# Optimization experiments

Hardware: AMD Instinct MI355X
Metric: run time of the kernel (lower is better)

The kernel has to match this reference:

```python
import jax, jax.numpy as jnp
import numpy as np

B, D = 32768, 1024


def setup_inputs() -> dict:
    key = jax.random.key(0)
    kx, k1, k2, k3 = jax.random.split(key, 4)
    x = jax.random.normal(kx, (B, D), dtype=jnp.float32)
    w1 = jax.random.normal(k1, (D, D), dtype=jnp.float32) * 0.1
    w2 = jax.random.normal(k2, (D, D), dtype=jnp.float32) * 0.1
    w3 = jax.random.normal(k3, (D, D), dtype=jnp.float32) * 0.1
    return {"x": x, "w1": w1, "w2": w2, "w3": w3}


def reference(x, w1, w2, w3):
    # Order 1: plain dense projection
    r1 = jnp.matmul(x, w1)  # [B, D]

    dim = x.shape[1]
    k = int(dim * 0.1)
    # Select top-k facets by mean |x| over the batch
    _, idx = jax.lax.top_k(jnp.abs(x).mean(axis=0), k)  # [k]
    mask = jnp.zeros((dim,), dtype=x.dtype).at[idx].set(1.0)  # [D]

    x_sparse = x * mask  # [B, D], zero outside active facets
    # Order 2: masked matmul, gated elementwise by the sparse input
    r2 = jnp.matmul(x_sparse, w2) * x_sparse
    # Order 3: masked matmul squared, gated elementwise
    r3 = jnp.square(jnp.matmul(x_sparse, w3)) * x_sparse
    return (r1, r2, r3)
```

## Files before the change

kernel.cpp:

```cpp
#include <hip/hip_runtime.h>
#include <hip/hip_bf16.h>
#include <stdint.h>

#define B_ROWS 32768
#define DIM    1024
#define KACT   102
#define KPAD   104

typedef short bf16x8 __attribute__((ext_vector_type(8)));
typedef unsigned short u16x8 __attribute__((ext_vector_type(8)));
typedef float f32x4  __attribute__((ext_vector_type(4)));

__device__ __forceinline__ unsigned short f2bf(float f) {
  union { float f; unsigned u; } v; v.f = f;
  unsigned u = v.u;
  unsigned r = u + 0x7fffu + ((u >> 16) & 1u);
  return (unsigned short)(r >> 16);
}
__device__ __forceinline__ float bfasf(unsigned hi16) {
  union { unsigned u; float f; } v; v.u = hi16;
  return v.f;
}

#define GLDS(g, l) __builtin_amdgcn_global_load_lds( \
    (__attribute__((address_space(1))) void*)(g),    \
    (__attribute__((address_space(3))) void*)(l), 16, 0, 0)

__global__ __launch_bounds__(256) void k_convw(
    const float* __restrict__ x, const float* __restrict__ w1,
    unsigned short* __restrict__ xb, unsigned short* __restrict__ w1t,
    float* __restrict__ partial) {
  const int t = threadIdx.x;
  if (blockIdx.x < 512) {
    const int c0 = t * 4;
    const size_t base = (size_t)blockIdx.x * 64 * DIM;
    float s0 = 0.f, s1 = 0.f, s2 = 0.f, s3 = 0.f;
    #pragma unroll 4
    for (int j = 0; j < 64; ++j) {
      size_t off = base + (size_t)j * DIM + c0;
      float4 v = *(const float4*)(x + off);
      s0 += fabsf(v.x); s1 += fabsf(v.y); s2 += fabsf(v.z); s3 += fabsf(v.w);
      ushort4 o;
      o.x = f2bf(v.x); o.y = f2bf(v.y); o.z = f2bf(v.z); o.w = f2bf(v.w);
      *(ushort4*)(xb + off) = o;
    }
    float4 p; p.x = s0; p.y = s1; p.z = s2; p.w = s3;
    *(float4*)(partial + (size_t)blockIdx.x * DIM + c0) = p;
  } else {
    __shared__ unsigned short tile[64][65];
    const int b  = blockIdx.x - 512;
    const int bx = b & 15;
    const int by = b >> 4;
    for (int e = t; e < 64 * 64; e += 256) {
      int r = e >> 6, c = e & 63;
      tile[r][c] = f2bf(w1[(size_t)(by * 64 + r) * DIM + bx * 64 + c]);
    }
    __syncthreads();
    for (int e = t; e < 64 * 64; e += 256) {
      int c = e >> 6, r = e & 63;
      w1t[(size_t)(bx * 64 + c) * DIM + by * 64 + r] = tile[r][c];
    }
  }
}

__global__ __launch_bounds__(128) void k_reduce1(const float* __restrict__ partial,
                                                 float* __restrict__ p2) {
  const int c  = (blockIdx.x & 7) * 128 + threadIdx.x;
  const int ks = blockIdx.x >> 3;
  float s = 0.f;
  #pragma unroll 8
  for (int p = ks * 64; p < ks * 64 + 64; ++p) s += partial[(size_t)p * DIM + c];
  p2[ks * DIM + c] = s;
}

__global__ __launch_bounds__(1024) void k_sel(const float* __restrict__ p2,
                                              int* __restrict__ act,
                                              int* __restrict__ cmap) {
  __shared__ double sv[DIM];
  __shared__ int wcnt[16];
  const int d = threadIdx.x;
  {
    double s = 0.0;
    #pragma unroll
    for (int ks = 0; ks < 8; ++ks) s += (double)p2[ks * DIM + d];
    sv[d] = s;
  }
  __syncthreads();
  const double sd = sv[d];
  int rank = 0;
  for (int j = 0; j < DIM; ++j) {
    double s = sv[j];
    rank += (s > sd || (s == sd && j < d)) ? 1 : 0;
  }
  const int f = (rank < KACT) ? 1 : 0;
  unsigned long long m = __ballot(f != 0);
  const int lane = d & 63, w = d >> 6;
  if (lane == 0) wcnt[w] = __popcll(m);
  __syncthreads();
  int off = 0;
  for (int i = 0; i < w; ++i) off += wcnt[i];
  int pos = off + __popcll(m & ((1ull << lane) - 1ull));
  cmap[d] = f ? pos : -1;
  if (f) act[pos] = d;
}

__global__ __launch_bounds__(128) void k_wsub(const float* __restrict__ w2,
                                              const float* __restrict__ w3,
                                              const int* __restrict__ act,
                                              float* __restrict__ W2sub,
                                              float* __restrict__ W3sub) {
  const int i = blockIdx.x;
  const int j = threadIdx.x;
  if (j >= KPAD) return;
  float v2 = 0.f, v3 = 0.f;
  if (i < KACT && j < KACT) {
    size_t o = (size_t)act[i] * DIM + act[j];
    v2 = w2[o]; v3 = w3[o];
  }
  W2sub[i * KPAD + j] = v2;
  W3sub[i * KPAD + j] = v3;
}

#define VMW8 asm volatile("s_waitcnt vmcnt(8)" ::: "memory")
#define VMW4 asm volatile("s_waitcnt vmcnt(4)" ::: "memory")
#define VMW0 asm volatile("s_waitcnt vmcnt(0)" ::: "memory")
#define NOP_ (void)0

#define STAGE_A(KT) do { \
  GLDS(Abase + (size_t)sr0 * 1024 + (KT) * 32 + sc0 * 8, &Asl[((KT)&3)*8192 + p0*8]); \
  GLDS(Abase + (size_t)sr1 * 1024 + (KT) * 32 + sc1 * 8, &Asl[((KT)&3)*8192 + p1*8]); \
} while (0)
#define STAGE_B(KT) do { \
  GLDS(Bbase + (size_t)sr0 * 1024 + (KT) * 32 + sc0 * 8, &Bsl[((KT)&3)*8192 + p0*8]); \
  GLDS(Bbase + (size_t)sr1 * 1024 + (KT) * 32 + sc1 * 8, &Bsl[((KT)&3)*8192 + p1*8]); \
} while (0)

#define PH0(SLOT, STAGE_STMT) do { \
  _Pragma("unroll") for (int i = 0; i < 4; ++i) \
    areg[i] = *(const bf16x8*)(&Asl[(SLOT)*8192 + aoff0 + i * 512]); \
  _Pragma("unroll") for (int i = 0; i < 4; ++i) \
    breg[i] = *(const bf16x8*)(&Bsl[(SLOT)*8192 + boff0 + i * 512]); \
  STAGE_STMT; \
  __builtin_amdgcn_s_barrier(); \
  __builtin_amdgcn_s_setprio(1); \
  _Pragma("unroll") for (int mi = 0; mi < 4; ++mi) \
  _Pragma("unroll") for (int ni = 0; ni < 4; ++ni) \
    acc[mi][ni] = __builtin_amdgcn_mfma_f32_16x16x32_bf16(areg[mi], breg[ni], acc[mi][ni], 0, 0, 0); \
  __builtin_amdgcn_s_setprio(0); \
  __builtin_amdgcn_s_barrier(); \
} while (0)

#define PH1(SLOT, STAGE_STMT, WAIT_STMT) do { \
  _Pragma("unroll") for (int i = 0; i < 4; ++i) \
    areg[i] = *(const bf16x8*)(&Asl[(SLOT)*8192 + aoff0 + 2048 + i * 512]); \
  STAGE_STMT; \
  WAIT_STMT; \
  __builtin_amdgcn_s_barrier(); \
  __builtin_amdgcn_s_setprio(1); \
  _Pragma("unroll") for (int mi = 0; mi < 4; ++mi) \
  _Pragma("unroll") for (int ni = 0; ni < 4; ++ni) \
    acc[4 + mi][ni] = __builtin_amdgcn_mfma_f32_16x16x32_bf16(areg[mi], breg[ni], acc[4 + mi][ni], 0, 0, 0); \
  __builtin_amdgcn_s_setprio(0); \
  __builtin_amdgcn_s_barrier(); \
} while (0)

__global__ __launch_bounds__(512, 1) void k_gemm_r1(
    const unsigned short* __restrict__ A,
    const unsigned short* __restrict__ Bt,
    float* __restrict__ C) {
  __shared__ unsigned short Asl[4 * 8192];
  __shared__ unsigned short Bsl[4 * 8192];

  const int t    = threadIdx.x;
  const int lane = t & 63;
  const int wave = t >> 6;
  const int wm   = wave >> 2;
  const int wn   = wave & 3;
  const int la   = lane & 15;
  const int kg   = lane >> 4;
  const int kgx  = kg ^ ((la >> 1) & 3);

  const int swz  = (blockIdx.x & 7) * 64 + (blockIdx.x >> 3);
  const int brow = swz >> 2;
  const int bcol = swz & 3;

  const unsigned short* Abase = A  + (size_t)brow * 256 * 1024;
  const unsigned short* Bbase = Bt + (size_t)bcol * 256 * 1024;

  const int p0 = t, p1 = t + 512;
  const int q0 = p0 ^ ((p0 >> 3) & 3);
  const int q1 = p1 ^ ((p1 >> 3) & 3);
  const int sr0 = q0 >> 2, sc0 = q0 & 3;
  const int sr1 = q1 >> 2, sc1 = q1 & 3;

  const int aoff0 = (wm * 128 + la) * 32 + kgx * 8;
  const int boff0 = (wn * 64  + la) * 32 + kgx * 8;

  f32x4 acc[8][4];
  #pragma unroll
  for (int mi = 0; mi < 8; ++mi)
    #pragma unroll
    for (int ni = 0; ni < 4; ++ni)
      acc[mi][ni] = (f32x4){0.f, 0.f, 0.f, 0.f};

  bf16x8 areg[4], breg[4];

  STAGE_A(0); STAGE_B(0); STAGE_A(1); STAGE_B(1); STAGE_A(2); STAGE_B(2);
  VMW8;
  __builtin_amdgcn_s_barrier();

  for (int kt4 = 0; kt4 < 28; kt4 += 4) {
    PH0(0, STAGE_A(kt4 + 3)); PH1(0, STAGE_B(kt4 + 3), VMW8);
    PH0(1, STAGE_A(kt4 + 4)); PH1(1, STAGE_B(kt4 + 4), VMW8);
    PH0(2, STAGE_A(kt4 + 5)); PH1(2, STAGE_B(kt4 + 5), VMW8);
    PH0(3, STAGE_A(kt4 + 6)); PH1(3, STAGE_B(kt4 + 6), VMW8);
  }
  PH0(0, STAGE_A(31)); PH1(0, STAGE_B(31), VMW8);
  PH0(1, NOP_);        PH1(1, NOP_, VMW4);
  PH0(2, NOP_);        PH1(2, NOP_, VMW0);
  PH0(3, NOP_);        PH1(3, NOP_, NOP_);

  const int orow0 = brow * 256 + wm * 128 + (lane >> 4) * 4;
  const int ocol0 = bcol * 256 + wn * 64 + la;
  #pragma unroll
  for (int mi = 0; mi < 8; ++mi)
    #pragma unroll
    for (int ni = 0; ni < 4; ++ni)
      #pragma unroll
      for (int r = 0; r < 4; ++r)
        C[(size_t)(orow0 + mi * 16 + r) * DIM + ocol0 + ni * 16] = acc[mi][ni][r];
}

__global__ __launch_bounds__(512) void k_r23(
    const unsigned short* __restrict__ xb,
    const float* __restrict__ W2sub,
    const float* __restrict__ W3sub,
    const int* __restrict__ cmap,
    float* __restrict__ out2,
    float* __restrict__ out3) {
  __shared__ float W2s[KPAD * KPAD];
  __shared__ float W3s[KPAD * KPAD];
  __shared__ float xs[2][16 * KPAD];
  __shared__ float r2s[16 * KPAD];
  __shared__ float r3s[16 * KPAD];
  __shared__ int   cms[DIM];
  const int t    = threadIdx.x;
  const int row0 = blockIdx.x * 128;

  for (int e = t; e < KPAD * KPAD; e += 512) { W2s[e] = W2sub[e]; W3s[e] = W3sub[e]; }
  for (int e = t; e < DIM; e += 512) cms[e] = cmap[e];
  for (int e = t; e < 2 * 16 * KPAD; e += 512) ((float*)xs)[e] = 0.f;
  __syncthreads();

  const int  j   = t & 127;
  const int  rg  = (t >> 7) & 3;
  const bool jok = j < KACT;

  auto LOADR = [&](int ch, u16x8* ld) {
    const size_t base = (size_t)(row0 + ch * 16) * DIM;
    #pragma unroll
    for (int it = 0; it < 4; ++it) {
      int e = t + it * 512;
      int r = e >> 7, c8 = e & 127;
      ld[it] = *(const u16x8*)(xb + base + (size_t)r * DIM + c8 * 8);
    }
  };
  auto XSW = [&](int buf, const u16x8* ld) {
    #pragma unroll
    for (int it = 0; it < 4; ++it) {
      int e = t + it * 512;
      int r = e >> 7, c8 = e & 127;
      #pragma unroll
      for (int q = 0; q < 8; ++q) {
        int m = cms[c8 * 8 + q];
        if (m >= 0) xs[buf][r * KPAD + m] = bfasf(((unsigned)(unsigned short)ld[it][q]) << 16);
      }
    }
  };
  auto COMPUTE = [&](int buf) {
    if (jok) {
      float a2[4], a3[4];
      #pragma unroll
      for (int r = 0; r < 4; ++r) { a2[r] = 0.f; a3[r] = 0.f; }
      for (int i = 0; i < KPAD; i += 4) {
        float w2v[4], w3v[4];
        #pragma unroll
        for (int q = 0; q < 4; ++q) {
          w2v[q] = W2s[(i + q) * KPAD + j];
          w3v[q] = W3s[(i + q) * KPAD + j];
        }
        #pragma unroll
        for (int r = 0; r < 4; ++r) {
          f32x4 xv = *(const f32x4*)(&xs[buf][(rg * 4 + r) * KPAD + i]);
          a2[r] += xv[0] * w2v[0] + xv[1] * w2v[1] + xv[2] * w2v[2] + xv[3] * w2v[3];
          a3[r] += xv[0] * w3v[0] + xv[1] * w3v[1] + xv[2] * w3v[2] + xv[3] * w3v[3];
        }
      }
      #pragma unroll
      for (int r = 0; r < 4; ++r) {
        int rr = rg * 4 + r;
        float g = xs[buf][rr * KPAD + j];
        r2s[rr * KPAD + j] = a2[r] * g;
        r3s[rr * KPAD + j] = a3[r] * a3[r] * g;
      }
    }
  };
  auto WRITEOUT = [&](int ch) {
    const int r0 = row0 + ch * 16;
    const int c0 = (t & 255) * 4;
    const int rh = t >> 8;
    const int4 cm = *(const int4*)(&cms[c0]);
    #pragma unroll
    for (int k = 0; k < 8; ++k) {
      int r = rh + k * 2;
      const float* rr2 = &r2s[r * KPAD];
      const float* rr3 = &r3s[r * KPAD];
      float4 o2, o3;
      o2.x = (cm.x >= 0) ? rr2[cm.x] : 0.f;  o3.x = (cm.x >= 0) ? rr3[cm.x] : 0.f;
      o2.y = (cm.y >= 0) ? rr2[cm.y] : 0.f;  o3.y = (cm.y >= 0) ? rr3[cm.y] : 0.f;
      o2.z = (cm.z >= 0) ? rr2[cm.z] : 0.f;  o3.z = (cm.z >= 0) ? rr3[cm.z] : 0.f;
      o2.w = (cm.w >= 0) ? rr2[cm.w] : 0.f;  o3.w = (cm.w >= 0) ? rr3[cm.w] : 0.f;
      size_t oo = (size_t)(r0 + r) * DIM + c0;
      *(float4*)(out2 + oo) = o2;
      *(float4*)(out3 + oo) = o3;
    }
  };

  u16x8 ldA[4], ldB[4];
  LOADR(0, ldA);
  XSW(0, ldA);
  __syncthreads();
  for (int ch2 = 0; ch2 < 8; ch2 += 2) {
    if (ch2 + 1 < 8) LOADR(ch2 + 1, ldB);
    COMPUTE(0);
    __syncthreads();
    WRITEOUT(ch2);
    if (ch2 + 1 < 8) XSW(1, ldB);
    __syncthreads();
    if (ch2 + 2 < 8) LOADR(ch2 + 2, ldA);
    COMPUTE(1);
    __syncthreads();
    WRITEOUT(ch2 + 1);
    if (ch2 + 2 < 8) XSW(0, ldA);
    __syncthreads();
  }
}

extern "C" void kernel_launch(void* const* d_in, const int* in_sizes, int n_in,
                              void* d_out, int out_size, void* d_ws, size_t ws_size,
                              hipStream_t stream) {
  const float* x  = (const float*)d_in[0];
  const float* w1 = (const float*)d_in[1];
  const float* w2 = (const float*)d_in[2];
  const float* w3 = (const float*)d_in[3];

  float* out1 = (float*)d_out;
  float* out2 = out1 + (size_t)B_ROWS * DIM;
  float* out3 = out2 + (size_t)B_ROWS * DIM;

  char* ws = (char*)d_ws;
  unsigned short* xb     = (unsigned short*)ws;
  unsigned short* w1t    = (unsigned short*)(ws + 67108864);
  float*          partial= (float*)(ws + 69206016);
  float*          p2     = (float*)(ws + 71303168);
  int*            cmap   = (int*)(ws + 71335936);
  int*            act    = (int*)(ws + 71340032);
  float*          W2sub  = (float*)(ws + 71340544);
  float*          W3sub  = (float*)(ws + 71383808);

  k_convw   <<<dim3(768),  dim3(256),  0, stream>>>(x, w1, xb, w1t, partial);
  k_reduce1 <<<dim3(64),   dim3(128),  0, stream>>>(partial, p2);
  k_sel     <<<dim3(1),    dim3(1024), 0, stream>>>(p2, act, cmap);
  k_wsub    <<<dim3(KPAD), dim3(128),  0, stream>>>(w2, w3, act, W2sub, W3sub);
  k_gemm_r1 <<<dim3(512),  dim3(512),  0, stream>>>(xb, w1t, out1);
  k_r23     <<<dim3(256),  dim3(512),  0, stream>>>(xb, W2sub, W3sub, cmap, out2, out3);
}
```

Before: 252.8 us.

## Fold top-k selection and weight gather into extra blocks of the GEMM launch

Removes the separate reduce, select and weight-subset kernels. Their work now runs in 16 extra blocks appended to the r1 GEMM launch, coordinated by an atomic last-block counter that is reset in the conversion kernel. The intent is to drop three small serial launches and hide the selection work under the large GEMM. The cost is that the last aux block runs the O(D^2) rank pass and an O(D) prefix count on 512 threads, which may finish later than the GEMM. Shared memory is also grown to a single 128 KB array.

```diff
diff --git a/kernel.cpp b/kernel.cpp
--- a/kernel.cpp
+++ b/kernel.cpp
@@ -29,8 +29,9 @@
 __global__ __launch_bounds__(256) void k_convw(
     const float* __restrict__ x, const float* __restrict__ w1,
     unsigned short* __restrict__ xb, unsigned short* __restrict__ w1t,
-    float* __restrict__ partial) {
+    float* __restrict__ partial, int* __restrict__ ctr) {
   const int t = threadIdx.x;
+  if (blockIdx.x == 0 && t == 0) *ctr = 0;
   if (blockIdx.x < 512) {
     const int c0 = t * 4;
     const size_t base = (size_t)blockIdx.x * 64 * DIM;
@@ -61,64 +62,6 @@
       w1t[(size_t)(bx * 64 + c) * DIM + by * 64 + r] = tile[r][c];
     }
   }
-}
-
-__global__ __launch_bounds__(128) void k_reduce1(const float* __restrict__ partial,
-                                                 float* __restrict__ p2) {
-  const int c  = (blockIdx.x & 7) * 128 + threadIdx.x;
-  const int ks = blockIdx.x >> 3;
-  float s = 0.f;
-  #pragma unroll 8
-  for (int p = ks * 64; p < ks * 64 + 64; ++p) s += partial[(size_t)p * DIM + c];
-  p2[ks * DIM + c] = s;
-}
-
-__global__ __launch_bounds__(1024) void k_sel(const float* __restrict__ p2,
-                                              int* __restrict__ act,
-                                              int* __restrict__ cmap) {
-  __shared__ double sv[DIM];
-  __shared__ int wcnt[16];
-  const int d = threadIdx.x;
-  {
-    double s = 0.0;
-    #pragma unroll
-    for (int ks = 0; ks < 8; ++ks) s += (double)p2[ks * DIM + d];
-    sv[d] = s;
-  }
-  __syncthreads();
-  const double sd = sv[d];
-  int rank = 0;
-  for (int j = 0; j < DIM; ++j) {
-    double s = sv[j];
-    rank += (s > sd || (s == sd && j < d)) ? 1 : 0;
-  }
-  const int f = (rank < KACT) ? 1 : 0;
-  unsigned long long m = __ballot(f != 0);
-  const int lane = d & 63, w = d >> 6;
-  if (lane == 0) wcnt[w] = __popcll(m);
-  __syncthreads();
-  int off = 0;
-  for (int i = 0; i < w; ++i) off += wcnt[i];
-  int pos = off + __popcll(m & ((1ull << lane) - 1ull));
-  cmap[d] = f ? pos : -1;
-  if (f) act[pos] = d;
-}
-
-__global__ __launch_bounds__(128) void k_wsub(const float* __restrict__ w2,
-                                              const float* __restrict__ w3,
-                                              const int* __restrict__ act,
-                                              float* __restrict__ W2sub,
-                                              float* __restrict__ W3sub) {
-  const int i = blockIdx.x;
-  const int j = threadIdx.x;
-  if (j >= KPAD) return;
-  float v2 = 0.f, v3 = 0.f;
-  if (i < KACT && j < KACT) {
-    size_t o = (size_t)act[i] * DIM + act[j];
-    v2 = w2[o]; v3 = w3[o];
-  }
-  W2sub[i * KPAD + j] = v2;
-  W3sub[i * KPAD + j] = v3;
 }
 
 #define VMW8 asm volatile("s_waitcnt vmcnt(8)" ::: "memory")
@@ -164,71 +107,145 @@
   __builtin_amdgcn_s_barrier(); \
 } while (0)
 
-__global__ __launch_bounds__(512, 1) void k_gemm_r1(
+__global__ __launch_bounds__(512, 1) void k_gemm_aux(
     const unsigned short* __restrict__ A,
     const unsigned short* __restrict__ Bt,
-    float* __restrict__ C) {
-  __shared__ unsigned short Asl[4 * 8192];
-  __shared__ unsigned short Bsl[4 * 8192];
-
-  const int t    = threadIdx.x;
-  const int lane = t & 63;
-  const int wave = t >> 6;
-  const int wm   = wave >> 2;
-  const int wn   = wave & 3;
-  const int la   = lane & 15;
-  const int kg   = lane >> 4;
-  const int kgx  = kg ^ ((la >> 1) & 3);
-
-  const int swz  = (blockIdx.x & 7) * 64 + (blockIdx.x >> 3);
-  const int brow = swz >> 2;
-  const int bcol = swz & 3;
-
-  const unsigned short* Abase = A  + (size_t)brow * 256 * 1024;
-  const unsigned short* Bbase = Bt + (size_t)bcol * 256 * 1024;
-
-  const int p0 = t, p1 = t + 512;
-  const int q0 = p0 ^ ((p0 >> 3) & 3);
-  const int q1 = p1 ^ ((p1 >> 3) & 3);
-  const int sr0 = q0 >> 2, sc0 = q0 & 3;
-  const int sr1 = q1 >> 2, sc1 = q1 & 3;
-
-  const int aoff0 = (wm * 128 + la) * 32 + kgx * 8;
-  const int boff0 = (wn * 64  + la) * 32 + kgx * 8;
-
-  f32x4 acc[8][4];
-  #pragma unroll
-  for (int mi = 0; mi < 8; ++mi)
-    #pragma unroll
-    for (int ni = 0; ni < 4; ++ni)
-      acc[mi][ni] = (f32x4){0.f, 0.f, 0.f, 0.f};
-
-  bf16x8 areg[4], breg[4];
-
-  STAGE_A(0); STAGE_B(0); STAGE_A(1); STAGE_B(1); STAGE_A(2); STAGE_B(2);
-  VMW8;
-  __builtin_amdgcn_s_barrier();
-
-  for (int kt4 = 0; kt4 < 28; kt4 += 4) {
-    PH0(0, STAGE_A(kt4 + 3)); PH1(0, STAGE_B(kt4 + 3), VMW8);
-    PH0(1, STAGE_A(kt4 + 4)); PH1(1, STAGE_B(kt4 + 4), VMW8);
-    PH0(2, STAGE_A(kt4 + 5)); PH1(2, STAGE_B(kt4 + 5), VMW8);
-    PH0(3, STAGE_A(kt4 + 6)); PH1(3, STAGE_B(kt4 + 6), VMW8);
+    float* __restrict__ C,
+    const float* __restrict__ partial,
+    float* __restrict__ p2,
+    const float* __restrict__ w2,
+    const float* __restrict__ w3,
+    int* __restrict__ ctr,
+    int* __restrict__ cmap,
+    float* __restrict__ W2sub,
+    float* __restrict__ W3sub) {
+  __shared__ __align__(16) char smem[131072];
+  const int t = threadIdx.x;
+
+  if (blockIdx.x < 512) {
+    unsigned short* Asl = (unsigned short*)smem;
+    unsigned short* Bsl = (unsigned short*)(smem + 65536);
+
+    const int lane = t & 63;
+    const int wave = t >> 6;
+    const int wm   = wave >> 2;
+    const int wn   = wave & 3;
+    const int la   = lane & 15;
+    const int kg   = lane >> 4;
+    const int kgx  = kg ^ ((la >> 1) & 3);
+
+    const int swz  = (blockIdx.x & 7) * 64 + (blockIdx.x >> 3);
+    const int brow = swz >> 2;
+    const int bcol = swz & 3;
+
+    const unsigned short* Abase = A  + (size_t)brow * 256 * 1024;
+    const unsigned short* Bbase = Bt + (size_t)bcol * 256 * 1024;
+
+    const int p0 = t, p1 = t + 512;
+    const int q0 = p0 ^ ((p0 >> 3) & 3);
+    const int q1 = p1 ^ ((p1 >> 3) & 3);
+    const int sr0 = q0 >> 2, sc0 = q0 & 3;
+    const int sr1 = q1 >> 2, sc1 = q1 & 3;
+
+    const int aoff0 = (wm * 128 + la) * 32 + kgx * 8;
+    const int boff0 = (wn * 64  + la) * 32 + kgx * 8;
+
+    f32x4 acc[8][4];
+    #pragma unroll
+    for (int mi = 0; mi < 8; ++mi)
+      #pragma unroll
+      for (int ni = 0; ni < 4; ++ni)
+        acc[mi][ni] = (f32x4){0.f, 0.f, 0.f, 0.f};
+
+    bf16x8 areg[4], breg[4];
+
+    STAGE_A(0); STAGE_B(0); STAGE_A(1); STAGE_B(1); STAGE_A(2); STAGE_B(2);
+    VMW8;
+    __builtin_amdgcn_s_barrier();
+
+    for (int kt4 = 0; kt4 < 28; kt4 += 4) {
+      PH0(0, STAGE_A(kt4 + 3)); PH1(0, STAGE_B(kt4 + 3), VMW8);
+      PH0(1, STAGE_A(kt4 + 4)); PH1(1, STAGE_B(kt4 + 4), VMW8);
+      PH0(2, STAGE_A(kt4 + 5)); PH1(2, STAGE_B(kt4 + 5), VMW8);
+      PH0(3, STAGE_A(kt4 + 6)); PH1(3, STAGE_B(kt4 + 6), VMW8);
+    }
+    PH0(0, STAGE_A(31)); PH1(0, STAGE_B(31), VMW8);
+    PH0(1, NOP_);        PH1(1, NOP_, VMW4);
+    PH0(2, NOP_);        PH1(2, NOP_, VMW0);
+    PH0(3, NOP_);        PH1(3, NOP_, NOP_);
+
+    const int orow0 = brow * 256 + wm * 128 + (lane >> 4) * 4;
+    const int ocol0 = bcol * 256 + wn * 64 + la;
+    #pragma unroll
+    for (int mi = 0; mi < 8; ++mi)
+      #pragma unroll
+      for (int ni = 0; ni < 4; ++ni)
+        #pragma unroll
+        for (int r = 0; r < 4; ++r)
+          C[(size_t)(orow0 + mi * 16 + r) * DIM + ocol0 + ni * 16] = acc[mi][ni][r];
+  } else {
+    const int a    = blockIdx.x - 512;
+    const int pair = a * 512 + t;
+    const int ks   = pair >> 10;
+    const int c    = pair & 1023;
+    {
+      float s = 0.f;
+      #pragma unroll 8
+      for (int p = ks * 64; p < ks * 64 + 64; ++p) s += partial[(size_t)p * DIM + c];
+      p2[ks * DIM + c] = s;
+    }
+    __threadfence();
+    __syncthreads();
+    __shared__ int lastFlag;
+    if (t == 0) lastFlag = (atomicAdd(ctr, 1) == 15);
+    __syncthreads();
+    if (!lastFlag) return;
+    __threadfence();
+
+    double* sv  = (double*)smem;
+    int*    af  = (int*)(smem + 8192);
+    int*    acts= (int*)(smem + 12288);
+    #pragma unroll
+    for (int h = 0; h < 2; ++h) {
+      int d = t + h * 512;
+      double s = 0.0;
+      #pragma unroll
+      for (int k8 = 0; k8 < 8; ++k8) s += (double)p2[k8 * DIM + d];
+      sv[d] = s;
+    }
+    __syncthreads();
+    #pragma unroll
+    for (int h = 0; h < 2; ++h) {
+      int d = t + h * 512;
+      const double sd = sv[d];
+      int rank = 0;
+      for (int j = 0; j < DIM; ++j) {
+        double s = sv[j];
+        rank += (s > sd || (s == sd && j < d)) ? 1 : 0;
+      }
+      af[d] = (rank < KACT) ? 1 : 0;
+    }
+    __syncthreads();
+    #pragma unroll
+    for (int h = 0; h < 2; ++h) {
+      int d = t + h * 512;
+      int f = af[d];
+      int pos = 0;
+      for (int j = 0; j < d; ++j) pos += af[j];
+      cmap[d] = f ? pos : -1;
+      if (f) acts[pos] = d;
+    }
+    __syncthreads();
+    for (int e = t; e < KPAD * KPAD; e += 512) {
+      int i = e / KPAD, j = e - i * KPAD;
+      float v2 = 0.f, v3 = 0.f;
+      if (i < KACT && j < KACT) {
+        size_t o = (size_t)acts[i] * DIM + acts[j];
+        v2 = w2[o]; v3 = w3[o];
+      }
+      W2sub[e] = v2; W3sub[e] = v3;
+    }
   }
-  PH0(0, STAGE_A(31)); PH1(0, STAGE_B(31), VMW8);
-  PH0(1, NOP_);        PH1(1, NOP_, VMW4);
-  PH0(2, NOP_);        PH1(2, NOP_, VMW0);
-  PH0(3, NOP_);        PH1(3, NOP_, NOP_);
-
-  const int orow0 = brow * 256 + wm * 128 + (lane >> 4) * 4;
-  const int ocol0 = bcol * 256 + wn * 64 + la;
-  #pragma unroll
-  for (int mi = 0; mi < 8; ++mi)
-    #pragma unroll
-    for (int ni = 0; ni < 4; ++ni)
-      #pragma unroll
-      for (int r = 0; r < 4; ++r)
-        C[(size_t)(orow0 + mi * 16 + r) * DIM + ocol0 + ni * 16] = acc[mi][ni][r];
 }
 
 __global__ __launch_bounds__(512) void k_r23(
@@ -364,14 +381,12 @@
   float*          partial= (float*)(ws + 69206016);
   float*          p2     = (float*)(ws + 71303168);
   int*            cmap   = (int*)(ws + 71335936);
-  int*            act    = (int*)(ws + 71340032);
+  int*            ctr    = (int*)(ws + 71340032);
   float*          W2sub  = (float*)(ws + 71340544);
   float*          W3sub  = (float*)(ws + 71383808);
 
-  k_convw   <<<dim3(768),  dim3(256),  0, stream>>>(x, w1, xb, w1t, partial);
-  k_reduce1 <<<dim3(64),   dim3(128),  0, stream>>>(partial, p2);
-  k_sel     <<<dim3(1),    dim3(1024), 0, stream>>>(p2, act, cmap);
-  k_wsub    <<<dim3(KPAD), dim3(128),  0, stream>>>(w2, w3, act, W2sub, W3sub);
-  k_gemm_r1 <<<dim3(512),  dim3(512),  0, stream>>>(xb, w1t, out1);
-  k_r23     <<<dim3(256),  dim3(512),  0, stream>>>(xb, W2sub, W3sub, cmap, out2, out3);
-}
+  k_convw    <<<dim3(768), dim3(256), 0, stream>>>(x, w1, xb, w1t, partial, ctr);
+  k_gemm_aux <<<dim3(528), dim3(512), 0, stream>>>(xb, w1t, out1, partial, p2,
+                                                   w2, w3, ctr, cmap, W2sub, W3sub);
+  k_r23      <<<dim3(256), dim3(512), 0, stream>>>(xb, W2sub, W3sub, cmap, out2, out3);
+}
```

After: 294.6 us. +16.5%, slower.
